# Performance work log

Hardware: AMD Instinct MI355X
Metric: run time of the kernel (lower is better)

## Reference

```python
import jax, jax.numpy as jnp
import numpy as np

# Grid / model constants (from cfg: scene_bbox [0,0,0,102.4,102.4,6.4], featmap_size=quant_size=0.4, n_input=5, batch=2)
B, N = 2, 300000
X, Y, Z, T = 256, 256, 16, 5
QUANT = np.array([0.4, 0.4, 0.4, 1.0], dtype=np.float32)
C_MID, N_CLASSES = 8, 1  # MinkUNet14 INIT_DIM=8, out=n_classes=1
KOFF = 3  # 3^4 = 81 kernel offsets of the first 4D sparse conv


def setup_inputs() -> dict:
    key = jax.random.key(0)
    ks = jax.random.split(key, 5)
    xyz = jax.random.uniform(ks[0], (B, N, 3), dtype=jnp.float32) * jnp.array([102.4, 102.4, 6.4], jnp.float32)
    t = jax.random.randint(ks[1], (B, N, 1), 0, T).astype(jnp.float32)
    points = jnp.concatenate([xyz, t], axis=-1)  # [B, N, 4] 4D point clouds (x,y,z,t)
    W0 = jax.random.normal(ks[2], (KOFF**4, 1, C_MID), jnp.float32) * 0.1  # per-offset GEMM weights
    b0 = jnp.zeros((C_MID,), jnp.float32)
    W1 = jax.random.normal(ks[3], (C_MID, N_CLASSES), jnp.float32) * 0.1  # pointwise head
    b1 = jnp.zeros((N_CLASSES,), jnp.float32)
    return {"points": points, "W0": W0, "b0": b0, "W1": W1, "b1": b1}


def _voxelize(points):
    """Quantize 4D points and unweighted-average per-voxel features (ME.TensorField.sparse())."""
    coords = jnp.floor(points / jnp.asarray(QUANT)).astype(jnp.int32)  # [B, N, 4]
    cx = jnp.clip(coords[..., 0], 0, X - 1)
    cy = jnp.clip(coords[..., 1], 0, Y - 1)
    cz = jnp.clip(coords[..., 2], 0, Z - 1)
    ct = jnp.clip(coords[..., 3], 0, T - 1)
    lin = ((cx * Y + cy) * Z + cz) * T + ct            # [B, N] linear voxel index
    lin = (lin + jnp.arange(B, dtype=jnp.int32)[:, None] * (X * Y * Z * T)).reshape(-1)
    feats = jnp.full((B * N,), 0.5, points.dtype)      # feats = 0.5 * ones(len(pcd), 1)
    nseg = B * X * Y * Z * T
    s = jax.ops.segment_sum(feats, lin, num_segments=nseg)
    cnt = jax.ops.segment_sum(jnp.ones_like(feats), lin, num_segments=nseg)
    occ = cnt > 0
    avg = jnp.where(occ, s / jnp.maximum(cnt, 1.0), 0.0)
    grid = avg.reshape(B, X, Y, Z, T, 1)               # densified sparse features (zeros at empty voxels)
    mask = occ.reshape(B, X, Y, Z, T, 1).astype(points.dtype)
    return grid, mask


def reference(points, W0, b0, W1, b1):
    grid, mask = _voxelize(points)
    # 4D generalized sparse conv (kernel 3^4), stride 1: out coords == in coords.
    # Densified form: shift-gather neighbors, GEMM with per-offset weights, accumulate, mask to occupied voxels.
    pad = jnp.pad(grid, ((0, 0), (1, 1), (1, 1), (1, 1), (1, 1), (0, 0)))
    out = jnp.zeros(grid.shape[:-1] + (C_MID,), grid.dtype)
    k = 0
    for dx in range(KOFF):
        for dy in range(KOFF):
            for dz in range(KOFF):
                for dt in range(KOFF):
                    nb = pad[:, dx:dx + X, dy:dy + Y, dz:dz + Z, dt:dt + T, :]  # [B,X,Y,Z,T,1]
                    out = out + nb @ W0[k]
                    k += 1
    out = jax.nn.relu((out + b0) * mask)
    out = (out @ W1 + b1) * mask                        # pointwise sparse conv to n_classes
    return jnp.moveaxis(out, -1, 1)                     # dense featmap [B, 1, X, Y, Z, T]
```

## Files before the change

kernel.cpp:

```cpp
#include <hip/hip_runtime.h>

#define XD 256
#define YD 256
#define ZD 16
#define TD 5
#define BD 2
#define NP 300000
#define CMID 8
#define VPB (XD * YD * ZD * TD)
#define NVOX (BD * VPB)
#define MAXPTS (BD * NP)

#define OCC8_BYTES (BD * XD * YD * ZD * 8)
#define OCC8_U128  (OCC8_BYTES / 16)
#define NCOL   (BD * XD * YD)

#define SCAT_BLOCKS ((MAXPTS + 255) / 256)
#define CONV_BLOCKS 4096
#define CTHR 256
#define QCAP 512

__global__ __launch_bounds__(256) void zero_kernel(uint4* __restrict__ occ) {
    int i = blockIdx.x * 256 + threadIdx.x;
    uint4 z = {0u, 0u, 0u, 0u};
    for (int j = i; j < OCC8_U128; j += 2048 * 256) occ[j] = z;
}

__global__ __launch_bounds__(256) void scatter_kernel(
    const float4* __restrict__ pts, unsigned char* __restrict__ occ8) {
    int i = blockIdx.x * 256 + threadIdx.x;
    if (i >= MAXPTS) return;
    float4 p = pts[i];
    int cx = min(max((int)floorf(p.x / 0.4f), 0), XD - 1);
    int cy = min(max((int)floorf(p.y / 0.4f), 0), YD - 1);
    int cz = min(max((int)floorf(p.z / 0.4f), 0), ZD - 1);
    int ct = min(max((int)floorf(p.w / 1.0f), 0), TD - 1);
    int b  = i / NP;
    unsigned a = (((unsigned)b << 23) | ((unsigned)cx << 15) |
                  ((unsigned)cy << 7) | ((unsigned)cz << 3) | (unsigned)ct);
    occ8[a] = 1;
}

__device__ __forceinline__ unsigned pack8(unsigned long long v) {
    v |= v >> 7;
    v |= v >> 14;
    v |= v >> 28;
    return (unsigned)v & 0xffu;
}

__global__ __launch_bounds__(256) void pack_kernel(
    const ulonglong2* __restrict__ occ16, unsigned short* __restrict__ pk) {
    int j = blockIdx.x * 256 + threadIdx.x;
    ulonglong2 v = occ16[j];
    pk[j] = (unsigned short)(pack8(v.x) | (pack8(v.y) << 8));
}

__global__ __launch_bounds__(CTHR) void conv_kernel(
    const ulonglong2* __restrict__ pk128,
    const float* __restrict__ W0,
    const float* __restrict__ b0,
    const float* __restrict__ W1,
    const float* __restrict__ b1,
    float4* __restrict__ out4) {
    __shared__ float w0s[81 * 12];
    __shared__ unsigned ccol[102 * 6];
    __shared__ unsigned short queue[QCAP];
    __shared__ float outt[32 * 80];
    __shared__ unsigned wsum[2];
    __shared__ float b0s[CMID];
    __shared__ float w1s[CMID];
    __shared__ float b1sv;

    int tid = threadIdx.x;
    int s   = blockIdx.x;
    int b   = s >> 11;
    int x   = (s >> 3) & 255;
    int ny0 = (s & 7) << 5;

    float4* ot4 = (float4*)outt;
    float4 zf = {0.f, 0.f, 0.f, 0.f};
    for (int j = tid; j < 640; j += CTHR) ot4[j] = zf;

    if (tid < 81) {
        const float4* src = (const float4*)(W0 + tid * CMID);
        *(float4*)&w0s[tid * 12]     = src[0];
        *(float4*)&w0s[tid * 12 + 4] = src[1];
    }
    if (tid < CMID) {
        b0s[tid] = b0[tid];
        w1s[tid] = W1[tid];
    }
    if (tid == 0) b1sv = b1[0];

    if (tid < 3 * 34) {
        int r   = tid / 34;
        int cyl = tid % 34;
        int nx  = x + r - 1;
        int cy  = ny0 + cyl - 1;
        bool valid = ((unsigned)nx < XD) && ((unsigned)cy < YD);
        ulonglong2 v = pk128[(b << 16) | ((nx & 255) << 8) | (cy & 255)];
        unsigned long long lo = valid ? v.x : 0ull;
        unsigned long long hi = valid ? v.y : 0ull;
        unsigned* c = &ccol[tid * 6];
        c[0] = 0u;
        c[1] = (unsigned)lo;
        c[2] = (unsigned)(lo >> 32);
        c[3] = (unsigned)hi;
        c[4] = (unsigned)(hi >> 32);
        c[5] = 0u;
    }
    __syncthreads();

    if (tid < 128) {
        unsigned w = ccol[(35 + (tid >> 2)) * 6 + 1 + (tid & 3)];
        int cnt = __popc(w);

        unsigned pre = (unsigned)cnt;
#pragma unroll
        for (int off = 1; off < 64; off <<= 1) {
            unsigned v = (unsigned)__shfl_up((int)pre, off, 64);
            if ((tid & 63) >= off) pre += v;
        }
        int wv = tid >> 6;
        if ((tid & 63) == 63) wsum[wv] = pre;
        __syncthreads();
        unsigned pos = ((wv == 1) ? wsum[0] : 0u) + pre - (unsigned)cnt;

        int cl = tid >> 2;
        int zb = (tid & 3) << 2;
        unsigned ww = w;
        while (ww) {
            int bi = __ffs(ww) - 1;
            ww &= ww - 1;
            int zz = zb + (bi >> 3);
            int tt = bi & 7;
            if (pos < QCAP)
                queue[pos] = (unsigned short)((cl << 7) | (zz << 3) | tt);
            ++pos;
        }
    } else {
        __syncthreads();
    }
    __syncthreads();
    unsigned qlen = wsum[0] + wsum[1];
    if (qlen > QCAP) qlen = QCAP;

    if (tid < (int)qlen) {
        int e  = queue[tid];
        int cl = e >> 7;
        int z  = (e >> 3) & 15;
        int t  = e & 7;

        int wi = (z + 3) >> 2;
        int sh = ((z + 3) & 3) * 8;

        unsigned long long mpA = 0ull;
        unsigned mpB = 0u;
#pragma unroll
        for (int dxi = 0; dxi < 3; ++dxi) {
#pragma unroll
            for (int dyi = 0; dyi < 3; ++dyi) {
                const unsigned* c = &ccol[(dxi * 34 + cl + dyi) * 6 + wi];
                unsigned lo32 = c[0];
                unsigned hi32 = c[1];
                unsigned w32 = (unsigned)(((((unsigned long long)hi32) << 32)
                                           | lo32) >> sh);
                unsigned qw = ((w32 & 0xffffffu) << 1) >> t;
                unsigned nine = (qw & 7u) | (((qw >> 8) & 7u) << 3) |
                                (((qw >> 16) & 7u) << 6);
                int c9 = dxi * 3 + dyi;
                if (c9 < 7) mpA |= (unsigned long long)nine << (9 * c9);
                else if (c9 == 7) mpB |= nine;
                else mpB |= nine << 9;
            }
        }

        float4 h0 = zf, h1 = zf;
        while (mpA) {
            int j = __ffsll(mpA) - 1;
            mpA &= mpA - 1;
            const float4* row = (const float4*)&w0s[j * 12];
            h0 += row[0];
            h1 += row[1];
        }
        while (mpB) {
            int j = __ffs(mpB) - 1;
            mpB &= mpB - 1;
            const float4* row = (const float4*)&w0s[(63 + j) * 12];
            h0 += row[0];
            h1 += row[1];
        }

        float hc[CMID] = {h0.x, h0.y, h0.z, h0.w, h1.x, h1.y, h1.z, h1.w};
        float o = 0.0f;
#pragma unroll
        for (int c = 0; c < CMID; ++c) {
            float v = 0.5f * hc[c] + b0s[c];
            v = v > 0.0f ? v : 0.0f;
            o += v * w1s[c];
        }
        outt[cl * 80 + z * 5 + t] = o + b1sv;
    }
    __syncthreads();

    const float4* src = (const float4*)outt;
    float4* dst = out4 + ((size_t)b * (VPB / 4)) + (size_t)(x * YD + ny0) * 20;
    for (int j = tid; j < 640; j += CTHR) dst[j] = src[j];
}

extern "C" void kernel_launch(void* const* d_in, const int* in_sizes, int n_in,
                              void* d_out, int out_size, void* d_ws, size_t ws_size,
                              hipStream_t stream) {
    const float4* pts = (const float4*)d_in[0];
    const float* W0   = (const float*)d_in[1];
    const float* b0   = (const float*)d_in[2];
    const float* W1   = (const float*)d_in[3];
    const float* b1   = (const float*)d_in[4];
    unsigned char* occ8 = (unsigned char*)d_ws;
    unsigned short* pk  = (unsigned short*)((char*)d_ws + OCC8_BYTES);

    zero_kernel<<<2048, 256, 0, stream>>>((uint4*)occ8);
    scatter_kernel<<<SCAT_BLOCKS, 256, 0, stream>>>(pts, occ8);
    pack_kernel<<<OCC8_U128 / 256, 256, 0, stream>>>(
        (const ulonglong2*)occ8, pk);
    conv_kernel<<<CONV_BLOCKS, 256, 0, stream>>>(
        (const ulonglong2*)pk, W0, b0, W1, b1, (float4*)d_out);
}
```

Measured before the change: 39.84 us.

## Scatter occupancy directly into packed bitmask with atomicOr, drop pack kernel

Instead of writing one byte per voxel into an 8x-oversized byte grid and then packing it into bits in a separate kernel, the scatter kernel sets bits directly in a packed bitmask using atomicOr. This removes the large byte buffer, its zeroing traffic, and the pack kernel launch, shrinking the zero pass eightfold. In exchange, 600k scattered global atomics replace plain byte stores, and collisions on shared words may serialize.

```diff
diff --git a/kernel.cpp b/kernel.cpp
--- a/kernel.cpp
+++ b/kernel.cpp
@@ -11,23 +11,20 @@
 #define NVOX (BD * VPB)
 #define MAXPTS (BD * NP)
 
-#define OCC8_BYTES (BD * XD * YD * ZD * 8)
-#define OCC8_U128  (OCC8_BYTES / 16)
-#define NCOL   (BD * XD * YD)
+#define OCC_BYTES (BD * XD * YD * ZD)
+#define OCC_U128  (OCC_BYTES / 16)
 
 #define SCAT_BLOCKS ((MAXPTS + 255) / 256)
 #define CONV_BLOCKS 4096
 #define CTHR 256
 #define QCAP 512
 
-__global__ __launch_bounds__(256) void zero_kernel(uint4* __restrict__ occ) {
-    int i = blockIdx.x * 256 + threadIdx.x;
-    uint4 z = {0u, 0u, 0u, 0u};
-    for (int j = i; j < OCC8_U128; j += 2048 * 256) occ[j] = z;
+__global__ __launch_bounds__(256) void zero_occ_kernel(uint4* __restrict__ occ) {
+    occ[blockIdx.x * 256 + threadIdx.x] = uint4{0u, 0u, 0u, 0u};
 }
 
 __global__ __launch_bounds__(256) void scatter_kernel(
-    const float4* __restrict__ pts, unsigned char* __restrict__ occ8) {
+    const float4* __restrict__ pts, unsigned int* __restrict__ occ) {
     int i = blockIdx.x * 256 + threadIdx.x;
     if (i >= MAXPTS) return;
     float4 p = pts[i];
@@ -36,23 +33,9 @@
     int cz = min(max((int)floorf(p.z / 0.4f), 0), ZD - 1);
     int ct = min(max((int)floorf(p.w / 1.0f), 0), TD - 1);
     int b  = i / NP;
-    unsigned a = (((unsigned)b << 23) | ((unsigned)cx << 15) |
-                  ((unsigned)cy << 7) | ((unsigned)cz << 3) | (unsigned)ct);
-    occ8[a] = 1;
-}
-
-__device__ __forceinline__ unsigned pack8(unsigned long long v) {
-    v |= v >> 7;
-    v |= v >> 14;
-    v |= v >> 28;
-    return (unsigned)v & 0xffu;
-}
-
-__global__ __launch_bounds__(256) void pack_kernel(
-    const ulonglong2* __restrict__ occ16, unsigned short* __restrict__ pk) {
-    int j = blockIdx.x * 256 + threadIdx.x;
-    ulonglong2 v = occ16[j];
-    pk[j] = (unsigned short)(pack8(v.x) | (pack8(v.y) << 8));
+    unsigned idx8 = (((unsigned)b << 23) | ((unsigned)cx << 15) |
+                     ((unsigned)cy << 7) | ((unsigned)cz << 3) | (unsigned)ct);
+    atomicOr(&occ[idx8 >> 5], 1u << (idx8 & 31));
 }
 
 __global__ __launch_bounds__(CTHR) void conv_kernel(
@@ -216,13 +199,10 @@
     const float* b0   = (const float*)d_in[2];
     const float* W1   = (const float*)d_in[3];
     const float* b1   = (const float*)d_in[4];
-    unsigned char* occ8 = (unsigned char*)d_ws;
-    unsigned short* pk  = (unsigned short*)((char*)d_ws + OCC8_BYTES);
-
-    zero_kernel<<<2048, 256, 0, stream>>>((uint4*)occ8);
-    scatter_kernel<<<SCAT_BLOCKS, 256, 0, stream>>>(pts, occ8);
-    pack_kernel<<<OCC8_U128 / 256, 256, 0, stream>>>(
-        (const ulonglong2*)occ8, pk);
+    unsigned int* occ = (unsigned int*)d_ws;
+
+    zero_occ_kernel<<<OCC_U128 / 256, 256, 0, stream>>>((uint4*)occ);
+    scatter_kernel<<<SCAT_BLOCKS, 256, 0, stream>>>(pts, occ);
     conv_kernel<<<CONV_BLOCKS, 256, 0, stream>>>(
-        (const ulonglong2*)pk, W0, b0, W1, b1, (float4*)d_out);
-}
+        (const ulonglong2*)occ, W0, b0, W1, b1, (float4*)d_out);
+}
```

After: 51.26 us. 1.29x slower.
